# Kernel tuning notes

Hardware: AMD Instinct MI355X
Metric: run time of the kernel (lower is better)

The kernel has to match this reference:

```python
import jax, jax.numpy as jnp
import numpy as np

B, S, D, H, E, K = 8, 512, 512, 1024, 8, 2


def setup_inputs() -> dict:
    key = jax.random.key(0)
    ks = jax.random.split(key, 8)
    x = jax.random.normal(ks[0], (B, S, D), dtype=jnp.float32)
    mask = jax.random.randint(ks[1], (B, S), 0, 2, dtype=jnp.int32)
    # xavier-uniform gate weights (torch init.xavier_uniform_)
    lim_g = np.sqrt(6.0 / (D + E))
    w_gate = jax.random.uniform(ks[2], (D, E), minval=-lim_g, maxval=lim_g, dtype=jnp.float32)
    # per-expert MLP params (nn.Linear default: U(-1/sqrt(fan_in), 1/sqrt(fan_in)))
    lim1 = 1.0 / np.sqrt(D)
    lim2 = 1.0 / np.sqrt(H)
    W1 = jax.random.uniform(ks[3], (E, D, H), minval=-lim1, maxval=lim1, dtype=jnp.float32)
    b1 = jax.random.uniform(ks[4], (E, H), minval=-lim1, maxval=lim1, dtype=jnp.float32)
    W2 = jax.random.uniform(ks[5], (E, H, D), minval=-lim2, maxval=lim2, dtype=jnp.float32)
    b2 = jax.random.uniform(ks[6], (E, D), minval=-lim2, maxval=lim2, dtype=jnp.float32)
    return {"x": x, "mask": mask, "w_gate": w_gate, "W1": W1, "b1": b1, "W2": W2, "b2": b2}


def reference(x, mask, w_gate, W1, b1, W2, b2):
    # --- top-k gating (noisy_gating=False path; loss = 0) ---
    logits = jnp.einsum('bsd,de->bse', x, w_gate)              # [B,S,E]
    top_vals, top_idx = jax.lax.top_k(logits, K)               # [B,S,K]
    top_gates = jax.nn.softmax(top_vals, axis=-1)              # softmax over top-k only
    onehot = jax.nn.one_hot(top_idx, E, dtype=x.dtype)         # [B,S,K,E]
    gates = jnp.einsum('bsk,bske->bse', top_gates, onehot)     # scatter to dense gates
    gates = gates * mask[..., None].astype(x.dtype)            # self.clean(gates, mask)
    # --- per-expert 2-layer MLP, combined with gates ---
    # dense formulation: zero gates contribute zero, identical math to dispatch/combine
    h = jax.nn.relu(jnp.einsum('bsd,edh->besh', x, W1) + b1[None, :, None, :])
    out = jnp.einsum('besh,eho->beso', h, W2) + b2[None, :, None, :]
    y = jnp.einsum('bse,beso->bso', gates, out)
    # dropout is identity in eval; residual add
    return y + x
```

## Files before the change

kernel.cpp:

```cpp
#include <hip/hip_runtime.h>
#include <cmath>

#define B_ 8
#define S_ 512
#define D_ 512
#define H_ 1024
#define E_ 8
#define NT_ (B_*S_)
#define TM 16
#define MAXTILE 40

typedef __attribute__((ext_vector_type(8))) short short8v;
typedef __attribute__((ext_vector_type(4))) float f32x4;

__device__ inline unsigned short f2bf(float f) {
    union { float f; unsigned u; } a; a.f = f;
    unsigned u = a.u;
    return (unsigned short)((u + 0x7FFF + ((u >> 16) & 1)) >> 16);
}
__device__ inline float bf2f(unsigned short u) {
    union { unsigned u; float f; } a; a.u = ((unsigned)u) << 16; return a.f;
}


__global__ __launch_bounds__(256) void prep_fused(
    const float* __restrict__ x, const int* __restrict__ mask,
    const float* __restrict__ wg,
    const float* __restrict__ W1, const float* __restrict__ W2,
    float* __restrict__ out, unsigned short* __restrict__ xbf,
    uchar2* __restrict__ tokE, float2* __restrict__ tokG,
    unsigned short* __restrict__ W1S, unsigned short* __restrict__ W2S)
{
    const int tid = threadIdx.x, wave = tid >> 6, lane = tid & 63;
    const int bid = blockIdx.x;

    if (bid < 1024) {
        const int t = bid * 4 + wave;
        const float4* xr = (const float4*)(x + ((size_t)t << 9));
        const float4 v0 = xr[lane];
        const float4 v1 = xr[lane + 64];
        float4* orow = (float4*)(out + ((size_t)t << 9));
        orow[lane] = v0; orow[lane + 64] = v1;
        union { unsigned short u[4]; uint2 w; } pa, pb;
        pa.u[0]=f2bf(v0.x); pa.u[1]=f2bf(v0.y); pa.u[2]=f2bf(v0.z); pa.u[3]=f2bf(v0.w);
        pb.u[0]=f2bf(v1.x); pb.u[1]=f2bf(v1.y); pb.u[2]=f2bf(v1.z); pb.u[3]=f2bf(v1.w);
        uint2* xrow = (uint2*)(xbf + ((size_t)t << 9));
        xrow[lane] = pa.w; xrow[lane + 64] = pb.w;

        float acc[E_];
#pragma unroll
        for (int e = 0; e < E_; ++e) acc[e] = 0.f;
        const int d0 = lane * 4;
#pragma unroll
        for (int dd = 0; dd < 4; ++dd) {
            const float xa = (&v0.x)[dd], xb = (&v1.x)[dd];
            const float4 wa0 = *(const float4*)(wg + (size_t)(d0 + dd) * 8);
            const float4 wa1 = *(const float4*)(wg + (size_t)(d0 + dd) * 8 + 4);
            const float4 wb0 = *(const float4*)(wg + (size_t)(256 + d0 + dd) * 8);
            const float4 wb1 = *(const float4*)(wg + (size_t)(256 + d0 + dd) * 8 + 4);
            acc[0] += xa * wa0.x + xb * wb0.x;
            acc[1] += xa * wa0.y + xb * wb0.y;
            acc[2] += xa * wa0.z + xb * wb0.z;
            acc[3] += xa * wa0.w + xb * wb0.w;
            acc[4] += xa * wa1.x + xb * wb1.x;
            acc[5] += xa * wa1.y + xb * wb1.y;
            acc[6] += xa * wa1.z + xb * wb1.z;
            acc[7] += xa * wa1.w + xb * wb1.w;
        }
#pragma unroll
        for (int e = 0; e < E_; ++e) {
            float v = acc[e];
#pragma unroll
            for (int off = 32; off > 0; off >>= 1) v += __shfl_xor(v, off, 64);
            acc[e] = v;
        }
        if (lane == 0) {
            if (mask[t] != 0) {
                int i0 = 0; float v0m = acc[0];
#pragma unroll
                for (int e = 1; e < E_; ++e) if (acc[e] > v0m) { v0m = acc[e]; i0 = e; }
                int i1 = -1; float v1m = -INFINITY;
#pragma unroll
                for (int e = 0; e < E_; ++e) if (e != i0 && acc[e] > v1m) { v1m = acc[e]; i1 = e; }
                const float ex = __expf(v1m - v0m);
                const float denom = 1.f + ex;
                tokE[t] = make_uchar2((unsigned char)i0, (unsigned char)i1);
                tokG[t] = make_float2(1.f / denom, ex / denom);
            } else {
                tokE[t] = make_uchar2(255, 255);
            }
        }
        return;
    }

    const int isW2 = (bid >= 1536);
    const int q = ((bid - (isW2 ? 1536 : 1024)) << 2) | wave;
    const int e = q >> 8, rem = q & 255;
    const int g = lane >> 4, m = lane & 15;
    const float* base; unsigned short* dstB; int stride, K32, Fq, kidx;
    if (!isW2) {
        Fq = rem >> 4; kidx = rem & 15;
        stride = H_; K32 = 16; base = W1; dstB = W1S;
    } else {
        Fq = rem >> 5; kidx = rem & 31;
        stride = D_; K32 = 32; base = W2; dstB = W2S;
    }
    const int k = kidx * 32 + g * 8;
    const float* src = base + ((size_t)e << 19) + (size_t)k * stride + Fq * 64 + m;
    float v[4][8];
#pragma unroll
    for (int j = 0; j < 8; ++j) {
#pragma unroll
        for (int c = 0; c < 4; ++c)
            v[c][j] = src[(size_t)j * stride + c * 16];
    }
#pragma unroll
    for (int c = 0; c < 4; ++c) {
        union { unsigned short u[8]; uint4 qv; } p;
#pragma unroll
        for (int j = 0; j < 8; ++j) p.u[j] = f2bf(v[c][j]);
        unsigned short* dst = dstB + ((size_t)e << 19)
                            + ((size_t)((Fq * 4 + c) * K32 + kidx) << 9) + lane * 8;
        *(uint4*)dst = p.qv;
    }
}

__global__ __launch_bounds__(256) void build1_kernel(
    const uchar2* __restrict__ tokE,
    ushort2* __restrict__ locs, int* __restrict__ blockCnt)
{
    __shared__ int waveTot[4][E_];
    const int tid = threadIdx.x, lane = tid & 63, wave = tid >> 6;
    const int t = blockIdx.x * 256 + tid;
    const uchar2 ee = tokE[t];
    int scan_pre[E_];
#pragma unroll
    for (int e = 0; e < E_; ++e) {
        const int orig = (ee.x == e) + (ee.y == e);
        int v = orig;
#pragma unroll
        for (int off = 1; off < 64; off <<= 1) {
            const int o = __shfl_up(v, off, 64);
            if (lane >= off) v += o;
        }
        scan_pre[e] = v - orig;
        if (lane == 63) waveTot[wave][e] = v;
    }
    __syncthreads();
    int loc0 = 0, loc1 = 0;
#pragma unroll
    for (int e = 0; e < E_; ++e) {
        int add = 0;
#pragma unroll
        for (int w = 0; w < 4; ++w) if (w < wave) add += waveTot[w][e];
        const int pre = scan_pre[e] + add;
        if (ee.x == e) loc0 = pre;
        if (ee.y == e) loc1 = pre;
    }
    if (tid < E_)
        blockCnt[blockIdx.x * E_ + tid] =
            waveTot[0][tid] + waveTot[1][tid] + waveTot[2][tid] + waveTot[3][tid];
    if (ee.x != 255)
        locs[t] = make_ushort2((unsigned short)loc0, (unsigned short)loc1);
}

__global__ __launch_bounds__(256) void build2_kernel(
    const uchar2* __restrict__ tokE, const float2* __restrict__ tokG,
    const ushort2* __restrict__ locs, const int* __restrict__ blockCnt,
    int* __restrict__ counts, int* __restrict__ lists, float* __restrict__ gvals,
    ushort2* __restrict__ tokSlot)
{
    __shared__ int bc[16][E_];
    const int tid = threadIdx.x;
    const int b = blockIdx.x;
    if (tid < 16 * E_) bc[tid >> 3][tid & 7] = blockCnt[tid];
    __syncthreads();
    if (b == 0 && tid < E_) {
        int s = 0;
#pragma unroll
        for (int bb = 0; bb < 16; ++bb) s += bc[bb][tid];
        counts[tid] = s;
    }
    const int t = b * 256 + tid;
    const uchar2 ee = tokE[t];
    if (ee.x == 255) return;
    int base0 = 0, base1 = 0, ex0 = 0, ex1 = 0, cum = 0;
#pragma unroll
    for (int e = 0; e < E_; ++e) {
        int boff = 0, tot = 0;
#pragma unroll
        for (int bb = 0; bb < 16; ++bb) {
            const int v = bc[bb][e];
            tot += v;
            if (bb < b) boff += v;
        }
        if (ee.x == e) { base0 = boff; ex0 = cum; }
        if (ee.y == e) { base1 = boff; ex1 = cum; }
        cum += tot;
    }
    const ushort2 lc = locs[t];
    const float2 gg = tokG[t];
    const int s0 = ee.x * NT_ + base0 + lc.x;
    const int s1 = ee.y * NT_ + base1 + lc.y;
    lists[s0] = t; gvals[s0] = gg.x;
    lists[s1] = t; gvals[s1] = gg.y;
    tokSlot[t] = make_ushort2((unsigned short)(ex0 + base0 + lc.x),
                              (unsigned short)(ex1 + base1 + lc.y));
}

__global__ __launch_bounds__(256) void stage1_kernel(
    const unsigned short* __restrict__ xbf,
    const unsigned short* __restrict__ W1S, const float* __restrict__ b1,
    const int* __restrict__ counts, const int* __restrict__ lists,
    unsigned short* __restrict__ Hbuf)
{
    __shared__ int tks[32];
    __shared__ unsigned short Xs[32 * D_];
    char* XsC = (char*)Xs;

    const int bid = blockIdx.x;
    const int e  = bid & 7;
    const int nb = (bid >> 3) & 3;
    const int ti = bid >> 5;
    const int n_e = counts[e];
    const int t0 = ti << 5;
    if (t0 >= n_e) return;
    int off = 0;
#pragma unroll
    for (int i = 0; i < E_; ++i) if (i < e) off += counts[i];
    const int mact = min(32, n_e - t0);
    const int tid = threadIdx.x;
    if (tid < 32) tks[tid] = lists[e * NT_ + t0 + min(tid, mact - 1)];
    __syncthreads();

#pragma unroll
    for (int j = 0; j < 8; ++j) {
        const int idx = tid + j * 256;
        const int row = idx >> 6, c = idx & 63;
        const uint4 v = *(const uint4*)(xbf + ((size_t)tks[row] << 9) + c * 8);
        *(uint4*)(XsC + ((row * 1024 + c * 16) ^ ((row & 7) << 4))) = v;
    }
    __syncthreads();

    const int wave = tid >> 6, lane = tid & 63, m = lane & 15, g = lane >> 4;
    const int colbase = nb * 256 + wave * 64;

    const int aoff0 = m * 1024 + (g << 4);
    const int aoff1 = (16 + m) * 1024 + (g << 4);
    const int aswz  = (m & 7) << 4;
    const unsigned short* Bb = W1S + ((size_t)e << 19)
                             + ((size_t)(nb * 16 + wave * 4) << 13) + (lane << 3);

    f32x4 acc[2][4];
#pragma unroll
    for (int i = 0; i < 2; ++i)
#pragma unroll
        for (int f = 0; f < 4; ++f) acc[i][f] = (f32x4){0.f, 0.f, 0.f, 0.f};

#pragma unroll 2
    for (int kk = 0; kk < 16; ++kk) {
        const short8v a0 = *(const short8v*)(XsC + ((aoff0 + (kk << 6)) ^ aswz));
        const short8v a1 = *(const short8v*)(XsC + ((aoff1 + (kk << 6)) ^ aswz));
        const short8v b0  = *(const short8v*)(Bb + (kk << 9));
        const short8v b1v = *(const short8v*)(Bb + (1 << 13) + (kk << 9));
        const short8v b2v = *(const short8v*)(Bb + (2 << 13) + (kk << 9));
        const short8v b3  = *(const short8v*)(Bb + (3 << 13) + (kk << 9));
        acc[0][0] = __builtin_amdgcn_mfma_f32_16x16x32_bf16(a0, b0,  acc[0][0], 0, 0, 0);
        acc[1][0] = __builtin_amdgcn_mfma_f32_16x16x32_bf16(a1, b0,  acc[1][0], 0, 0, 0);
        acc[0][1] = __builtin_amdgcn_mfma_f32_16x16x32_bf16(a0, b1v, acc[0][1], 0, 0, 0);
        acc[1][1] = __builtin_amdgcn_mfma_f32_16x16x32_bf16(a1, b1v, acc[1][1], 0, 0, 0);
        acc[0][2] = __builtin_amdgcn_mfma_f32_16x16x32_bf16(a0, b2v, acc[0][2], 0, 0, 0);
        acc[1][2] = __builtin_amdgcn_mfma_f32_16x16x32_bf16(a1, b2v, acc[1][2], 0, 0, 0);
        acc[0][3] = __builtin_amdgcn_mfma_f32_16x16x32_bf16(a0, b3,  acc[0][3], 0, 0, 0);
        acc[1][3] = __builtin_amdgcn_mfma_f32_16x16x32_bf16(a1, b3,  acc[1][3], 0, 0, 0);
    }

#pragma unroll
    for (int f = 0; f < 4; ++f) {
        const int col = colbase + f * 16 + m;
        const float bias = b1[(e << 10) + col];
#pragma unroll
        for (int i = 0; i < 2; ++i)
#pragma unroll
            for (int r = 0; r < 4; ++r) {
                const int row = i * 16 + g * 4 + r;
                if (row < mact)
                    Hbuf[((size_t)(off + t0 + row) << 10) + col] =
                        f2bf(fmaxf(acc[i][f][r] + bias, 0.f));
            }
    }
}

__global__ __launch_bounds__(256) void stage2y_kernel(
    const unsigned short* __restrict__ Hbuf,
    const unsigned short* __restrict__ W2S, const float* __restrict__ b2,
    const int* __restrict__ counts, unsigned short* __restrict__ Ybuf)
{
    __shared__ unsigned short Hs[32 * 512];
    char* HsC = (char*)Hs;

    const int bid = blockIdx.x;
    const int e  = bid & 7;
    const int nb = (bid >> 3) & 1;
    const int ti = bid >> 4;
    const int n_e = counts[e];
    const int t0 = ti << 5;
    if (t0 >= n_e) return;
    int off = 0;
#pragma unroll
    for (int i = 0; i < E_; ++i) if (i < e) off += counts[i];
    const int mact = min(32, n_e - t0);

    const int tid = threadIdx.x;
    const int wave = tid >> 6, lane = tid & 63, m = lane & 15, g = lane >> 4;
    const int colbase = nb * 256 + wave * 64;
    const int aswz = (m & 7) << 4;

    const unsigned short* Bb = W2S + ((size_t)e << 19)
                             + ((size_t)(nb * 16 + wave * 4) << 14) + (lane << 3);

    f32x4 acc[2][4];
#pragma unroll
    for (int i = 0; i < 2; ++i)
#pragma unroll
        for (int f = 0; f < 4; ++f) acc[i][f] = (f32x4){0.f, 0.f, 0.f, 0.f};

#pragma unroll
    for (int phase = 0; phase < 2; ++phase) {
        if (phase) __syncthreads();
#pragma unroll
        for (int j = 0; j < 8; ++j) {
            const int idx = tid + j * 256;
            const int row = idx >> 6, c = idx & 63;
            const uint4 v = *(const uint4*)(Hbuf + ((size_t)(off + t0 + row) << 10)
                                            + phase * 512 + c * 8);
            *(uint4*)(HsC + ((row * 1024 + c * 16) ^ ((row & 7) << 4))) = v;
        }
        __syncthreads();

#pragma unroll 2
        for (int kk = 0; kk < 16; ++kk) {
            const short8v a0 = *(const short8v*)(HsC + ((m * 1024 + (kk << 6) + (g << 4)) ^ aswz));
            const short8v a1 = *(const short8v*)(HsC + (((16 + m) * 1024 + (kk << 6) + (g << 4)) ^ aswz));
            const int kg = phase * 16 + kk;
            const short8v b0  = *(const short8v*)(Bb + (kg << 9));
            const short8v b1v = *(const short8v*)(Bb + (1 << 14) + (kg << 9));
            const short8v b2v = *(const short8v*)(Bb + (2 << 14) + (kg << 9));
            const short8v b3  = *(const short8v*)(Bb + (3 << 14) + (kg << 9));
            acc[0][0] = __builtin_amdgcn_mfma_f32_16x16x32_bf16(b0,  a0, acc[0][0], 0, 0, 0);
            acc[1][0] = __builtin_amdgcn_mfma_f32_16x16x32_bf16(b0,  a1, acc[1][0], 0, 0, 0);
            acc[0][1] = __builtin_amdgcn_mfma_f32_16x16x32_bf16(b1v, a0, acc[0][1], 0, 0, 0);
            acc[1][1] = __builtin_amdgcn_mfma_f32_16x16x32_bf16(b1v, a1, acc[1][1], 0, 0, 0);
            acc[0][2] = __builtin_amdgcn_mfma_f32_16x16x32_bf16(b2v, a0, acc[0][2], 0, 0, 0);
            acc[1][2] = __builtin_amdgcn_mfma_f32_16x16x32_bf16(b2v, a1, acc[1][2], 0, 0, 0);
            acc[0][3] = __builtin_amdgcn_mfma_f32_16x16x32_bf16(b3,  a0, acc[0][3], 0, 0, 0);
            acc[1][3] = __builtin_amdgcn_mfma_f32_16x16x32_bf16(b3,  a1, acc[1][3], 0, 0, 0);
        }
    }

#pragma unroll
    for (int f = 0; f < 4; ++f) {
        const int c0 = colbase + f * 16 + 4 * g;
        const float4 bv = *(const float4*)(b2 + (e << 9) + c0);
#pragma unroll
        for (int i = 0; i < 2; ++i) {
            const int token = i * 16 + m;
            if (token < mact) {
                const unsigned lo = (unsigned)f2bf(acc[i][f][0] + bv.x)
                                  | ((unsigned)f2bf(acc[i][f][1] + bv.y) << 16);
                const unsigned hi = (unsigned)f2bf(acc[i][f][2] + bv.z)
                                  | ((unsigned)f2bf(acc[i][f][3] + bv.w) << 16);
                *(uint2*)(Ybuf + ((size_t)(off + t0 + token) << 9) + c0) = make_uint2(lo, hi);
            }
        }
    }
}

__global__ __launch_bounds__(256) void combine_kernel(
    const uchar2* __restrict__ tokE, const float2* __restrict__ tokG,
    const ushort2* __restrict__ tokSlot, const unsigned short* __restrict__ Ybuf,
    float* __restrict__ out)
{
    const int tid = threadIdx.x, wave = tid >> 6, lane = tid & 63;
    const int t = blockIdx.x * 4 + wave;
    const uchar2 ee = tokE[t];
    if (ee.x == 255) return;
    const float2 gg = tokG[t];
    const ushort2 ss = tokSlot[t];
    const unsigned short* y0 = Ybuf + ((size_t)ss.x << 9);
    const unsigned short* y1 = Ybuf + ((size_t)ss.y << 9);
    float4* orow = (float4*)(out + ((size_t)t << 9));
#pragma unroll
    for (int h = 0; h < 2; ++h) {
        const int idx = lane + h * 64;
        float4 o = orow[idx];
        const uint2 a = *(const uint2*)(y0 + 4 * idx);
        const uint2 b = *(const uint2*)(y1 + 4 * idx);
        o.x += gg.x * bf2f((unsigned short)(a.x & 0xFFFF)) + gg.y * bf2f((unsigned short)(b.x & 0xFFFF));
        o.y += gg.x * bf2f((unsigned short)(a.x >> 16))    + gg.y * bf2f((unsigned short)(b.x >> 16));
        o.z += gg.x * bf2f((unsigned short)(a.y & 0xFFFF)) + gg.y * bf2f((unsigned short)(b.y & 0xFFFF));
        o.w += gg.x * bf2f((unsigned short)(a.y >> 16))    + gg.y * bf2f((unsigned short)(b.y >> 16));
        orow[idx] = o;
    }
}

__global__ __launch_bounds__(256) void stage2_kernel(
    const unsigned short* __restrict__ Hbuf,
    const unsigned short* __restrict__ W2S, const float* __restrict__ b2,
    const int* __restrict__ counts, const int* __restrict__ lists,
    const float* __restrict__ gvals, float* __restrict__ out)
{
    const int bid = blockIdx.x;
    const int e  = bid & 7;
    const int nb = (bid >> 3) & 1;
    const int ti = bid >> 4;
    const int n_e = counts[e];
    const int t0 = ti << 5;
    if (t0 >= n_e) return;
    int off = 0;
#pragma unroll
    for (int i = 0; i < E_; ++i) if (i < e) off += counts[i];
    const int mact = min(32, n_e - t0);
    __shared__ int tks[32];
    __shared__ float gsh[32];
    const int tid = threadIdx.x;
    if (tid < 32) {
        const int idx = min(tid, mact - 1);
        tks[tid] = lists[e * NT_ + t0 + idx];
        gsh[tid] = gvals[e * NT_ + t0 + idx];
    }
    __syncthreads();

    const int wave = tid >> 6, lane = tid & 63, m = lane & 15, g = lane >> 4;
    const int colbase = nb * 256 + wave * 64;

    const unsigned short* a0p = Hbuf + ((size_t)(off + t0 + m) << 10) + (g << 3);
    const unsigned short* a1p = Hbuf + ((size_t)(off + t0 + 16 + m) << 10) + (g << 3);
    const unsigned short* Bb = W2S + ((size_t)e << 19)
                             + ((size_t)(nb * 16 + wave * 4) << 14) + (lane << 3);

    f32x4 acc[2][4];
#pragma unroll
    for (int i = 0; i < 2; ++i)
#pragma unroll
        for (int f = 0; f < 4; ++f) acc[i][f] = (f32x4){0.f, 0.f, 0.f, 0.f};

#pragma unroll 2
    for (int kk = 0; kk < 32; ++kk) {
        const short8v a0 = *(const short8v*)(a0p + (kk << 5));
        const short8v a1 = *(const short8v*)(a1p + (kk << 5));
        const short8v b0  = *(const short8v*)(Bb + (kk << 9));
        const short8v b1v = *(const short8v*)(Bb + (1 << 14) + (kk << 9));
        const short8v b2v = *(const short8v*)(Bb + (2 << 14) + (kk << 9));
        const short8v b3  = *(const short8v*)(Bb + (3 << 14) + (kk << 9));
        acc[0][0] = __builtin_amdgcn_mfma_f32_16x16x32_bf16(a0, b0,  acc[0][0], 0, 0, 0);
        acc[1][0] = __builtin_amdgcn_mfma_f32_16x16x32_bf16(a1, b0,  acc[1][0], 0, 0, 0);
        acc[0][1] = __builtin_amdgcn_mfma_f32_16x16x32_bf16(a0, b1v, acc[0][1], 0, 0, 0);
        acc[1][1] = __builtin_amdgcn_mfma_f32_16x16x32_bf16(a1, b1v, acc[1][1], 0, 0, 0);
        acc[0][2] = __builtin_amdgcn_mfma_f32_16x16x32_bf16(a0, b2v, acc[0][2], 0, 0, 0);
        acc[1][2] = __builtin_amdgcn_mfma_f32_16x16x32_bf16(a1, b2v, acc[1][2], 0, 0, 0);
        acc[0][3] = __builtin_amdgcn_mfma_f32_16x16x32_bf16(a0, b3,  acc[0][3], 0, 0, 0);
        acc[1][3] = __builtin_amdgcn_mfma_f32_16x16x32_bf16(a1, b3,  acc[1][3], 0, 0, 0);
    }

#pragma unroll
    for (int f = 0; f < 4; ++f) {
        const int col = colbase + f * 16 + m;
        const float bias = b2[(e << 9) + col];
#pragma unroll
        for (int i = 0; i < 2; ++i)
#pragma unroll
            for (int r = 0; r < 4; ++r) {
                const int row = i * 16 + g * 4 + r;
                if (row < mact)
                    atomicAdd(out + ((size_t)tks[row] << 9) + col,
                              (acc[i][f][r] + bias) * gsh[row]);
            }
    }
}


__global__ __launch_bounds__(256) void gating_kernel(
    const float* __restrict__ x, const int* __restrict__ mask,
    const float* __restrict__ wg, int* __restrict__ counts,
    int* __restrict__ lists, float* __restrict__ gvals)
{
    const int wave = threadIdx.x >> 6;
    const int lane = threadIdx.x & 63;
    const int t = blockIdx.x * 4 + wave;
    const float* xr = x + (size_t)t * D_;
    float acc[E_];
#pragma unroll
    for (int e = 0; e < E_; ++e) acc[e] = 0.f;
    for (int d = lane; d < D_; d += 64) {
        const float xv = xr[d];
        const float* wr = wg + (size_t)d * E_;
#pragma unroll
        for (int e = 0; e < E_; ++e) acc[e] += xv * wr[e];
    }
#pragma unroll
    for (int e = 0; e < E_; ++e) {
        float v = acc[e];
#pragma unroll
        for (int off = 32; off > 0; off >>= 1) v += __shfl_down(v, off, 64);
        acc[e] = v;
    }
    if (lane == 0 && mask[t] != 0) {
        int i0 = 0; float v0 = acc[0];
#pragma unroll
        for (int e = 1; e < E_; ++e) if (acc[e] > v0) { v0 = acc[e]; i0 = e; }
        int i1 = -1; float v1 = -INFINITY;
#pragma unroll
        for (int e = 0; e < E_; ++e) if (e != i0 && acc[e] > v1) { v1 = acc[e]; i1 = e; }
        const float ex = __expf(v1 - v0);
        const float denom = 1.f + ex;
        const int p0 = atomicAdd(&counts[i0], 1);
        lists[i0 * NT_ + p0] = t; gvals[i0 * NT_ + p0] = 1.f / denom;
        const int p1 = atomicAdd(&counts[i1], 1);
        lists[i1 * NT_ + p1] = t; gvals[i1 * NT_ + p1] = ex / denom;
    }
}

__global__ __launch_bounds__(256) void init_out_kernel(
    const float* __restrict__ x, float* __restrict__ out)
{
    const size_t i = (size_t)blockIdx.x * blockDim.x + threadIdx.x;
    ((float4*)out)[i] = ((const float4*)x)[i];
}

__global__ __launch_bounds__(256) void transpose_cvt(
    const float* __restrict__ src, unsigned short* __restrict__ dst, int R, int C)
{
    __shared__ unsigned short t[64][72];
    const float* s = src + (size_t)blockIdx.z * R * C;
    unsigned short* d = dst + (size_t)blockIdx.z * R * C;
    const int r0 = blockIdx.y * 64, c0 = blockIdx.x * 64;
    const int tc = threadIdx.x & 63;
    const int tr = threadIdx.x >> 6;
#pragma unroll
    for (int i = 0; i < 16; ++i) {
        const int r = tr + i * 4;
        t[r][tc] = f2bf(s[(size_t)(r0 + r) * C + c0 + tc]);
    }
    __syncthreads();
    const int c = threadIdx.x >> 2;
    const int ch = threadIdx.x & 3;
#pragma unroll
    for (int half = 0; half < 2; ++half) {
        union { unsigned short u[8]; uint4 v; } p;
#pragma unroll
        for (int k = 0; k < 8; ++k) p.u[k] = t[ch * 16 + half * 8 + k][c];
        *(uint4*)(d + (size_t)(c0 + c) * R + r0 + ch * 16 + half * 8) = p.v;
    }
}

__global__ __launch_bounds__(256) void expert_mfma(
    const float* __restrict__ x,
    const unsigned short* __restrict__ W1T, const float* __restrict__ b1,
    const unsigned short* __restrict__ W2T, const float* __restrict__ b2,
    const int* __restrict__ counts, const int* __restrict__ lists,
    const float* __restrict__ gvals, float* __restrict__ out)
{
    __shared__ unsigned short Xs[TM * D_];
    __shared__ unsigned short Hs2[TM * H_];
    __shared__ int   tks[TM];
    __shared__ float gs[TM];

    const int bi = blockIdx.x;
    const int e = bi & 7;
    const int t0 = (bi >> 3) * TM;
    const int n = counts[e];
    if (t0 >= n) return;
    const int tid = threadIdx.x;
    const int mact = min(TM, n - t0);
    const int wave = tid >> 6;
    const int lane = tid & 63;
    const int m = lane & 15;
    const int g = lane >> 4;
    char* XsC = (char*)Xs;
    char* HsC = (char*)Hs2;

    if (tid < TM) {
        if (tid < mact) {
            tks[tid] = lists[e * NT_ + t0 + tid];
            gs[tid]  = gvals[e * NT_ + t0 + tid];
        } else { tks[tid] = 0; gs[tid] = 0.f; }
    }
    __syncthreads();

    for (int idx = tid; idx < TM * (D_ / 8); idx += 256) {
        const int mm = idx >> 6;
        const int c8 = idx & 63;
        union { unsigned short u[8]; uint4 v; } p;
        if (mm < mact) {
            const float4* xr = (const float4*)(x + (size_t)tks[mm] * D_);
            const float4 v0 = xr[c8 * 2], v1 = xr[c8 * 2 + 1];
            p.u[0]=f2bf(v0.x); p.u[1]=f2bf(v0.y); p.u[2]=f2bf(v0.z); p.u[3]=f2bf(v0.w);
            p.u[4]=f2bf(v1.x); p.u[5]=f2bf(v1.y); p.u[6]=f2bf(v1.z); p.u[7]=f2bf(v1.w);
        } else {
            p.v = make_uint4(0, 0, 0, 0);
        }
        const int off = mm * (D_ * 2) + c8 * 16;
        *(uint4*)(XsC + (off ^ ((mm & 7) << 4))) = p.v;
    }
    __syncthreads();

    const int nbase = wave * 256;
    f32x4 acc1[16];
#pragma unroll
    for (int f = 0; f < 16; ++f) acc1[f] = (f32x4){0.f, 0.f, 0.f, 0.f};

    for (int k0 = 0; k0 < D_; k0 += 32) {
        const int aoff = m * (D_ * 2) + k0 * 2 + g * 16;
        const short8v a = *(const short8v*)(XsC + (aoff ^ ((m & 7) << 4)));
#pragma unroll
        for (int f = 0; f < 16; ++f) {
            const unsigned short* bp = W1T + (((size_t)(e << 10) + nbase + f * 16 + m) << 9) + k0 + g * 8;
            const short8v b = *(const short8v*)bp;
            acc1[f] = __builtin_amdgcn_mfma_f32_16x16x32_bf16(a, b, acc1[f], 0, 0, 0);
        }
    }
#pragma unroll
    for (int f = 0; f < 16; ++f) {
        const int nn = nbase + f * 16 + m;
        const float bias = b1[(e << 10) + nn];
#pragma unroll
        for (int r = 0; r < 4; ++r) {
            const int mm = g * 4 + r;
            const unsigned short hv = f2bf(fmaxf(acc1[f][r] + bias, 0.f));
            const int off = mm * (H_ * 2) + nn * 2;
            *(unsigned short*)(HsC + (off ^ ((mm & 7) << 4))) = hv;
        }
    }
    __syncthreads();

    const int obase = wave * 128;
    f32x4 acc2[8];
#pragma unroll
    for (int f = 0; f < 8; ++f) acc2[f] = (f32x4){0.f, 0.f, 0.f, 0.f};

    for (int k0 = 0; k0 < H_; k0 += 32) {
        const int aoff = m * (H_ * 2) + k0 * 2 + g * 16;
        const short8v a = *(const short8v*)(HsC + (aoff ^ ((m & 7) << 4)));
#pragma unroll
        for (int f = 0; f < 8; ++f) {
            const unsigned short* bp = W2T + (((size_t)(e << 9) + obase + f * 16 + m) << 10) + k0 + g * 8;
            const short8v b = *(const short8v*)bp;
            acc2[f] = __builtin_amdgcn_mfma_f32_16x16x32_bf16(a, b, acc2[f], 0, 0, 0);
        }
    }
#pragma unroll
    for (int f = 0; f < 8; ++f) {
        const int o = obase + f * 16 + m;
        const float bias = b2[(e << 9) + o];
#pragma unroll
        for (int r = 0; r < 4; ++r) {
            const int mm = g * 4 + r;
            const float gv = gs[mm];
            if (gv != 0.f)
                atomicAdd(out + (size_t)tks[mm] * D_ + o, (acc2[f][r] + bias) * gv);
        }
    }
}

__global__ __launch_bounds__(256) void expert_fp32(
    const float* __restrict__ x,
    const float* __restrict__ W1, const float* __restrict__ b1,
    const float* __restrict__ W2, const float* __restrict__ b2,
    const int* __restrict__ counts, const int* __restrict__ lists,
    const float* __restrict__ gvals, float* __restrict__ out)
{
    __shared__ float Xs[TM][D_];
    __shared__ float Hs3[TM][H_];
    __shared__ int   tks[TM];
    __shared__ float gs[TM];

    const int e  = blockIdx.y;
    const int n  = counts[e];
    const int t0 = blockIdx.x * TM;
    if (t0 >= n) return;
    const int tid  = threadIdx.x;
    const int mact = min(TM, n - t0);

    if (tid < TM) {
        if (tid < mact) {
            tks[tid] = lists[e * NT_ + t0 + tid];
            gs[tid]  = gvals[e * NT_ + t0 + tid];
        } else { tks[tid] = 0; gs[tid] = 0.f; }
    }
    __syncthreads();
    for (int idx = tid; idx < TM * (D_ / 4); idx += 256) {
        const int mm = idx >> 7, c = idx & 127;
        float4 v = make_float4(0.f, 0.f, 0.f, 0.f);
        if (mm < mact) v = ((const float4*)(x + (size_t)tks[mm] * D_))[c];
        ((float4*)&Xs[mm][0])[c] = v;
    }
    __syncthreads();
    const float* W1e = W1 + (size_t)e * D_ * H_;
    float acc[4][TM];
#pragma unroll
    for (int jj = 0; jj < 4; ++jj)
#pragma unroll
        for (int mm = 0; mm < TM; ++mm) acc[jj][mm] = 0.f;
    for (int d4 = 0; d4 < D_ / 4; ++d4) {
        float w[4][4];
#pragma unroll
        for (int dd = 0; dd < 4; ++dd) {
            const float* wp = W1e + (size_t)(d4 * 4 + dd) * H_ + tid;
#pragma unroll
            for (int jj = 0; jj < 4; ++jj) w[dd][jj] = wp[jj * 256];
        }
#pragma unroll
        for (int mm = 0; mm < TM; ++mm) {
            const float4 xv = ((const float4*)&Xs[mm][0])[d4];
            const float* xp = &xv.x;
#pragma unroll
            for (int dd = 0; dd < 4; ++dd)
#pragma unroll
                for (int jj = 0; jj < 4; ++jj)
                    acc[jj][mm] = fmaf(xp[dd], w[dd][jj], acc[jj][mm]);
        }
    }
#pragma unroll
    for (int jj = 0; jj < 4; ++jj) {
        const int j = jj * 256 + tid;
        const float bv = b1[e * H_ + j];
#pragma unroll
        for (int mm = 0; mm < TM; ++mm) Hs3[mm][j] = fmaxf(acc[jj][mm] + bv, 0.f);
    }
    __syncthreads();
    const float* W2e = W2 + (size_t)e * H_ * D_;
    float acc2[2][TM];
#pragma unroll
    for (int oo = 0; oo < 2; ++oo)
#pragma unroll
        for (int mm = 0; mm < TM; ++mm) acc2[oo][mm] = 0.f;
    for (int j4 = 0; j4 < H_ / 4; ++j4) {
        float w[4][2];
#pragma unroll
        for (int dd = 0; dd < 4; ++dd) {
            const float* wp = W2e + (size_t)(j4 * 4 + dd) * D_ + tid;
#pragma unroll
            for (int oo = 0; oo < 2; ++oo) w[dd][oo] = wp[oo * 256];
        }
#pragma unroll
        for (int mm = 0; mm < TM; ++mm) {
            const float4 hv = ((const float4*)&Hs3[mm][0])[j4];
            const float* hp = &hv.x;
#pragma unroll
            for (int dd = 0; dd < 4; ++dd)
#pragma unroll
                for (int oo = 0; oo < 2; ++oo)
                    acc2[oo][mm] = fmaf(hp[dd], w[dd][oo], acc2[oo][mm]);
        }
    }
#pragma unroll
    for (int oo = 0; oo < 2; ++oo) {
        const int o = oo * 256 + tid;
        const float bv = b2[e * D_ + o];
        for (int mm = 0; mm < mact; ++mm)
            atomicAdd(out + (size_t)tks[mm] * D_ + o, (acc2[oo][mm] + bv) * gs[mm]);
    }
}


extern "C" void kernel_launch(void* const* d_in, const int* in_sizes, int n_in,
                              void* d_out, int out_size, void* d_ws, size_t ws_size,
                              hipStream_t stream)
{
    const float* x    = (const float*)d_in[0];
    const int*   mask = (const int*)d_in[1];
    const float* wg   = (const float*)d_in[2];
    const float* W1   = (const float*)d_in[3];
    const float* b1   = (const float*)d_in[4];
    const float* W2   = (const float*)d_in[5];
    const float* b2   = (const float*)d_in[6];
    float* out = (float*)d_out;

    char* ws = (char*)d_ws;
    int*   counts = (int*)ws;
    int*   lists  = (int*)(ws + 256);
    float* gvals  = (float*)(ws + 256 + 131072);

    ushort2* tokSlot = (ushort2*)(ws + 0x42000);
    uchar2* tokE = (uchar2*)(ws + 0x48000);
    float2* tokG = (float2*)(ws + 0x50000);
    ushort2* locs = (ushort2*)(ws + 0x58000);
    int* blockCnt = (int*)(ws + 0x5C000);
    unsigned short* xbf  = (unsigned short*)(ws + 0x60000);
    unsigned short* W1Sa = (unsigned short*)(ws + 0x480000);
    unsigned short* W2Sa = (unsigned short*)(ws + 0xC80000);
    unsigned short* Hbuf = (unsigned short*)(ws + 0x1480000);
    unsigned short* Ybuf = (unsigned short*)(ws + 0x2500000);
    const size_t needA  = 0x2500000;
    const size_t needA2 = 0x2500000 + (size_t)8448 * 512 * 2;

    const size_t wt_bytes = (size_t)E_ * D_ * H_ * 2;
    const size_t needB = 524288 + 2 * wt_bytes;

    if (ws_size >= needA) {
        prep_fused<<<2048, 256, 0, stream>>>(x, mask, wg, W1, W2,
                                             out, xbf, tokE, tokG, W1Sa, W2Sa);
        build1_kernel<<<16, 256, 0, stream>>>(tokE, locs, blockCnt);
        build2_kernel<<<16, 256, 0, stream>>>(tokE, tokG, locs, blockCnt,
                                              counts, lists, gvals, tokSlot);
        stage1_kernel<<<MAXTILE * 4 * 8, 256, 0, stream>>>(xbf, W1Sa, b1, counts, lists, Hbuf);
        if (ws_size >= needA2) {
            stage2y_kernel<<<MAXTILE * 2 * 8, 256, 0, stream>>>(Hbuf, W2Sa, b2, counts, Ybuf);
            combine_kernel<<<1024, 256, 0, stream>>>(tokE, tokG, tokSlot, Ybuf, out);
        } else {
            stage2_kernel<<<MAXTILE * 2 * 8, 256, 0, stream>>>(Hbuf, W2Sa, b2, counts, lists, gvals, out);
        }
    } else if (ws_size >= needB) {
        unsigned short* W1T = (unsigned short*)(ws + 524288);
        unsigned short* W2T = (unsigned short*)(ws + 524288 + wt_bytes);
        hipMemsetAsync(counts, 0, E_ * sizeof(int), stream);
        gating_kernel<<<NT_ / 4, 256, 0, stream>>>(x, mask, wg, counts, lists, gvals);
        init_out_kernel<<<(NT_ * D_) / 4 / 256, 256, 0, stream>>>(x, out);
        transpose_cvt<<<dim3(H_ / 64, D_ / 64, E_), 256, 0, stream>>>(W1, W1T, D_, H_);
        transpose_cvt<<<dim3(D_ / 64, H_ / 64, E_), 256, 0, stream>>>(W2, W2T, H_, D_);
        expert_mfma<<<(NT_ / TM) * E_, 256, 0, stream>>>(x, W1T, b1, W2T, b2,
                                                         counts, lists, gvals, out);
    } else {
        hipMemsetAsync(counts, 0, E_ * sizeof(int), stream);
        gating_kernel<<<NT_ / 4, 256, 0, stream>>>(x, mask, wg, counts, lists, gvals);
        init_out_kernel<<<(NT_ * D_) / 4 / 256, 256, 0, stream>>>(x, out);
        expert_fp32<<<dim3(NT_ / TM, E_), 256, 0, stream>>>(x, W1, b1, W2, b2,
                                                            counts, lists, gvals, out);
    }
}
```

Measured before the change: 63.10 us.

## Merge routing build kernels and move residual copy into combine

Result: slower. 67.35 us (+6.7%).

```diff
diff --git a/kernel.cpp b/kernel.cpp
--- a/kernel.cpp
+++ b/kernel.cpp
@@ -27,7 +27,7 @@
     const float* __restrict__ x, const int* __restrict__ mask,
     const float* __restrict__ wg,
     const float* __restrict__ W1, const float* __restrict__ W2,
-    float* __restrict__ out, unsigned short* __restrict__ xbf,
+    unsigned short* __restrict__ xbf,
     uchar2* __restrict__ tokE, float2* __restrict__ tokG,
     unsigned short* __restrict__ W1S, unsigned short* __restrict__ W2S)
 {
@@ -39,8 +39,6 @@
         const float4* xr = (const float4*)(x + ((size_t)t << 9));
         const float4 v0 = xr[lane];
         const float4 v1 = xr[lane + 64];
-        float4* orow = (float4*)(out + ((size_t)t << 9));
-        orow[lane] = v0; orow[lane + 64] = v1;
         union { unsigned short u[4]; uint2 w; } pa, pb;
         pa.u[0]=f2bf(v0.x); pa.u[1]=f2bf(v0.y); pa.u[2]=f2bf(v0.z); pa.u[3]=f2bf(v0.w);
         pb.u[0]=f2bf(v1.x); pb.u[1]=f2bf(v1.y); pb.u[2]=f2bf(v1.z); pb.u[3]=f2bf(v1.w);
@@ -125,14 +123,41 @@
     }
 }
 
-__global__ __launch_bounds__(256) void build1_kernel(
-    const uchar2* __restrict__ tokE,
-    ushort2* __restrict__ locs, int* __restrict__ blockCnt)
-{
+__global__ __launch_bounds__(256) void build_kernel(
+    const uchar2* __restrict__ tokE, const float2* __restrict__ tokG,
+    int* __restrict__ counts, int* __restrict__ lists, float* __restrict__ gvals,
+    ushort2* __restrict__ tokSlot)
+{
+    __shared__ int wAll[4][E_];
+    __shared__ int wPre[4][E_];
     __shared__ int waveTot[4][E_];
     const int tid = threadIdx.x, lane = tid & 63, wave = tid >> 6;
-    const int t = blockIdx.x * 256 + tid;
-    const uchar2 ee = tokE[t];
+    const int b = blockIdx.x;
+
+    int hAll[E_], hPre[E_];
+#pragma unroll
+    for (int e = 0; e < E_; ++e) { hAll[e] = 0; hPre[e] = 0; }
+    for (int bb = 0; bb < 16; ++bb) {
+        const uchar2 e2 = tokE[bb * 256 + tid];
+#pragma unroll
+        for (int e = 0; e < E_; ++e) {
+            const int c = (e2.x == e) + (e2.y == e);
+            hAll[e] += c;
+            if (bb < b) hPre[e] += c;
+        }
+    }
+#pragma unroll
+    for (int e = 0; e < E_; ++e) {
+        int va = hAll[e], vp = hPre[e];
+#pragma unroll
+        for (int off = 32; off > 0; off >>= 1) {
+            va += __shfl_xor(va, off, 64);
+            vp += __shfl_xor(vp, off, 64);
+        }
+        if (lane == 0) { wAll[wave][e] = va; wPre[wave][e] = vp; }
+    }
+
+    const uchar2 ee = tokE[b * 256 + tid];
     int scan_pre[E_];
 #pragma unroll
     for (int e = 0; e < E_; ++e) {
@@ -147,65 +172,35 @@
         if (lane == 63) waveTot[wave][e] = v;
     }
     __syncthreads();
-    int loc0 = 0, loc1 = 0;
+
+    int tot[E_], boff[E_];
 #pragma unroll
     for (int e = 0; e < E_; ++e) {
-        int add = 0;
+        tot[e]  = wAll[0][e] + wAll[1][e] + wAll[2][e] + wAll[3][e];
+        boff[e] = wPre[0][e] + wPre[1][e] + wPre[2][e] + wPre[3][e];
+    }
+    if (b == 0 && tid < E_) counts[tid] = tot[tid];
+
+    if (ee.x == 255) return;
+    int we0 = 0, we1 = 0, ex0 = 0, ex1 = 0, cum = 0;
+#pragma unroll
+    for (int e = 0; e < E_; ++e) {
+        int add = boff[e];
 #pragma unroll
         for (int w = 0; w < 4; ++w) if (w < wave) add += waveTot[w][e];
         const int pre = scan_pre[e] + add;
-        if (ee.x == e) loc0 = pre;
-        if (ee.y == e) loc1 = pre;
-    }
-    if (tid < E_)
-        blockCnt[blockIdx.x * E_ + tid] =
-            waveTot[0][tid] + waveTot[1][tid] + waveTot[2][tid] + waveTot[3][tid];
-    if (ee.x != 255)
-        locs[t] = make_ushort2((unsigned short)loc0, (unsigned short)loc1);
-}
-
-__global__ __launch_bounds__(256) void build2_kernel(
-    const uchar2* __restrict__ tokE, const float2* __restrict__ tokG,
-    const ushort2* __restrict__ locs, const int* __restrict__ blockCnt,
-    int* __restrict__ counts, int* __restrict__ lists, float* __restrict__ gvals,
-    ushort2* __restrict__ tokSlot)
-{
-    __shared__ int bc[16][E_];
-    const int tid = threadIdx.x;
-    const int b = blockIdx.x;
-    if (tid < 16 * E_) bc[tid >> 3][tid & 7] = blockCnt[tid];
-    __syncthreads();
-    if (b == 0 && tid < E_) {
-        int s = 0;
-#pragma unroll
-        for (int bb = 0; bb < 16; ++bb) s += bc[bb][tid];
-        counts[tid] = s;
-    }
+        if (ee.x == e) { we0 = pre; ex0 = cum; }
+        if (ee.y == e) { we1 = pre; ex1 = cum; }
+        cum += tot[e];
+    }
+    const float2 gg = tokG[b * 256 + tid];
     const int t = b * 256 + tid;
-    const uchar2 ee = tokE[t];
-    if (ee.x == 255) return;
-    int base0 = 0, base1 = 0, ex0 = 0, ex1 = 0, cum = 0;
-#pragma unroll
-    for (int e = 0; e < E_; ++e) {
-        int boff = 0, tot = 0;
-#pragma unroll
-        for (int bb = 0; bb < 16; ++bb) {
-            const int v = bc[bb][e];
-            tot += v;
-            if (bb < b) boff += v;
-        }
-        if (ee.x == e) { base0 = boff; ex0 = cum; }
-        if (ee.y == e) { base1 = boff; ex1 = cum; }
-        cum += tot;
-    }
-    const ushort2 lc = locs[t];
-    const float2 gg = tokG[t];
-    const int s0 = ee.x * NT_ + base0 + lc.x;
-    const int s1 = ee.y * NT_ + base1 + lc.y;
+    const int s0 = ee.x * NT_ + we0;
+    const int s1 = ee.y * NT_ + we1;
     lists[s0] = t; gvals[s0] = gg.x;
     lists[s1] = t; gvals[s1] = gg.y;
-    tokSlot[t] = make_ushort2((unsigned short)(ex0 + base0 + lc.x),
-                              (unsigned short)(ex1 + base1 + lc.y));
+    tokSlot[t] = make_ushort2((unsigned short)(ex0 + we0),
+                              (unsigned short)(ex1 + we1));
 }
 
 __global__ __launch_bounds__(256) void stage1_kernel(
@@ -377,6 +372,7 @@
 }
 
 __global__ __launch_bounds__(256) void combine_kernel(
+    const float* __restrict__ x,
     const uchar2* __restrict__ tokE, const float2* __restrict__ tokG,
     const ushort2* __restrict__ tokSlot, const unsigned short* __restrict__ Ybuf,
     float* __restrict__ out)
@@ -384,16 +380,21 @@
     const int tid = threadIdx.x, wave = tid >> 6, lane = tid & 63;
     const int t = blockIdx.x * 4 + wave;
     const uchar2 ee = tokE[t];
-    if (ee.x == 255) return;
+    const float4* xrow = (const float4*)(x + ((size_t)t << 9));
+    float4* orow = (float4*)(out + ((size_t)t << 9));
+    if (ee.x == 255) {
+        orow[lane] = xrow[lane];
+        orow[lane + 64] = xrow[lane + 64];
+        return;
+    }
     const float2 gg = tokG[t];
     const ushort2 ss = tokSlot[t];
     const unsigned short* y0 = Ybuf + ((size_t)ss.x << 9);
     const unsigned short* y1 = Ybuf + ((size_t)ss.y << 9);
-    float4* orow = (float4*)(out + ((size_t)t << 9));
 #pragma unroll
     for (int h = 0; h < 2; ++h) {
         const int idx = lane + h * 64;
-        float4 o = orow[idx];
+        float4 o = xrow[idx];
         const uint2 a = *(const uint2*)(y0 + 4 * idx);
         const uint2 b = *(const uint2*)(y1 + 4 * idx);
         o.x += gg.x * bf2f((unsigned short)(a.x & 0xFFFF)) + gg.y * bf2f((unsigned short)(b.x & 0xFFFF));
@@ -401,81 +402,6 @@
         o.z += gg.x * bf2f((unsigned short)(a.y & 0xFFFF)) + gg.y * bf2f((unsigned short)(b.y & 0xFFFF));
         o.w += gg.x * bf2f((unsigned short)(a.y >> 16))    + gg.y * bf2f((unsigned short)(b.y >> 16));
         orow[idx] = o;
-    }
-}
-
-__global__ __launch_bounds__(256) void stage2_kernel(
-    const unsigned short* __restrict__ Hbuf,
-    const unsigned short* __restrict__ W2S, const float* __restrict__ b2,
-    const int* __restrict__ counts, const int* __restrict__ lists,
-    const float* __restrict__ gvals, float* __restrict__ out)
-{
-    const int bid = blockIdx.x;
-    const int e  = bid & 7;
-    const int nb = (bid >> 3) & 1;
-    const int ti = bid >> 4;
-    const int n_e = counts[e];
-    const int t0 = ti << 5;
-    if (t0 >= n_e) return;
-    int off = 0;
-#pragma unroll
-    for (int i = 0; i < E_; ++i) if (i < e) off += counts[i];
-    const int mact = min(32, n_e - t0);
-    __shared__ int tks[32];
-    __shared__ float gsh[32];
-    const int tid = threadIdx.x;
-    if (tid < 32) {
-        const int idx = min(tid, mact - 1);
-        tks[tid] = lists[e * NT_ + t0 + idx];
-        gsh[tid] = gvals[e * NT_ + t0 + idx];
-    }
-    __syncthreads();
-
-    const int wave = tid >> 6, lane = tid & 63, m = lane & 15, g = lane >> 4;
-    const int colbase = nb * 256 + wave * 64;
-
-    const unsigned short* a0p = Hbuf + ((size_t)(off + t0 + m) << 10) + (g << 3);
-    const unsigned short* a1p = Hbuf + ((size_t)(off + t0 + 16 + m) << 10) + (g << 3);
-    const unsigned short* Bb = W2S + ((size_t)e << 19)
-                             + ((size_t)(nb * 16 + wave * 4) << 14) + (lane << 3);
-
-    f32x4 acc[2][4];
-#pragma unroll
-    for (int i = 0; i < 2; ++i)
-#pragma unroll
-        for (int f = 0; f < 4; ++f) acc[i][f] = (f32x4){0.f, 0.f, 0.f, 0.f};
-
-#pragma unroll 2
-    for (int kk = 0; kk < 32; ++kk) {
-        const short8v a0 = *(const short8v*)(a0p + (kk << 5));
-        const short8v a1 = *(const short8v*)(a1p + (kk << 5));
-        const short8v b0  = *(const short8v*)(Bb + (kk << 9));
-        const short8v b1v = *(const short8v*)(Bb + (1 << 14) + (kk << 9));
-        const short8v b2v = *(const short8v*)(Bb + (2 << 14) + (kk << 9));
-        const short8v b3  = *(const short8v*)(Bb + (3 << 14) + (kk << 9));
-        acc[0][0] = __builtin_amdgcn_mfma_f32_16x16x32_bf16(a0, b0,  acc[0][0], 0, 0, 0);
-        acc[1][0] = __builtin_amdgcn_mfma_f32_16x16x32_bf16(a1, b0,  acc[1][0], 0, 0, 0);
-        acc[0][1] = __builtin_amdgcn_mfma_f32_16x16x32_bf16(a0, b1v, acc[0][1], 0, 0, 0);
-        acc[1][1] = __builtin_amdgcn_mfma_f32_16x16x32_bf16(a1, b1v, acc[1][1], 0, 0, 0);
-        acc[0][2] = __builtin_amdgcn_mfma_f32_16x16x32_bf16(a0, b2v, acc[0][2], 0, 0, 0);
-        acc[1][2] = __builtin_amdgcn_mfma_f32_16x16x32_bf16(a1, b2v, acc[1][2], 0, 0, 0);
-        acc[0][3] = __builtin_amdgcn_mfma_f32_16x16x32_bf16(a0, b3,  acc[0][3], 0, 0, 0);
-        acc[1][3] = __builtin_amdgcn_mfma_f32_16x16x32_bf16(a1, b3,  acc[1][3], 0, 0, 0);
-    }
-
-#pragma unroll
-    for (int f = 0; f < 4; ++f) {
-        const int col = colbase + f * 16 + m;
-        const float bias = b2[(e << 9) + col];
-#pragma unroll
-        for (int i = 0; i < 2; ++i)
-#pragma unroll
-            for (int r = 0; r < 4; ++r) {
-                const int row = i * 16 + g * 4 + r;
-                if (row < mact)
-                    atomicAdd(out + ((size_t)tks[row] << 9) + col,
-                              (acc[i][f][r] + bias) * gsh[row]);
-            }
     }
 }
 
@@ -785,32 +711,23 @@
     ushort2* tokSlot = (ushort2*)(ws + 0x42000);
     uchar2* tokE = (uchar2*)(ws + 0x48000);
     float2* tokG = (float2*)(ws + 0x50000);
-    ushort2* locs = (ushort2*)(ws + 0x58000);
-    int* blockCnt = (int*)(ws + 0x5C000);
     unsigned short* xbf  = (unsigned short*)(ws + 0x60000);
     unsigned short* W1Sa = (unsigned short*)(ws + 0x480000);
     unsigned short* W2Sa = (unsigned short*)(ws + 0xC80000);
     unsigned short* Hbuf = (unsigned short*)(ws + 0x1480000);
     unsigned short* Ybuf = (unsigned short*)(ws + 0x2500000);
-    const size_t needA  = 0x2500000;
     const size_t needA2 = 0x2500000 + (size_t)8448 * 512 * 2;
 
     const size_t wt_bytes = (size_t)E_ * D_ * H_ * 2;
     const size_t needB = 524288 + 2 * wt_bytes;
 
-    if (ws_size >= needA) {
+    if (ws_size >= needA2) {
         prep_fused<<<2048, 256, 0, stream>>>(x, mask, wg, W1, W2,
-                                             out, xbf, tokE, tokG, W1Sa, W2Sa);
-        build1_kernel<<<16, 256, 0, stream>>>(tokE, locs, blockCnt);
-        build2_kernel<<<16, 256, 0, stream>>>(tokE, tokG, locs, blockCnt,
-                                              counts, lists, gvals, tokSlot);
+                                             xbf, tokE, tokG, W1Sa, W2Sa);
+        build_kernel<<<16, 256, 0, stream>>>(tokE, tokG, counts, lists, gvals, tokSlot);
         stage1_kernel<<<MAXTILE * 4 * 8, 256, 0, stream>>>(xbf, W1Sa, b1, counts, lists, Hbuf);
-        if (ws_size >= needA2) {
-            stage2y_kernel<<<MAXTILE * 2 * 8, 256, 0, stream>>>(Hbuf, W2Sa, b2, counts, Ybuf);
-            combine_kernel<<<1024, 256, 0, stream>>>(tokE, tokG, tokSlot, Ybuf, out);
-        } else {
-            stage2_kernel<<<MAXTILE * 2 * 8, 256, 0, stream>>>(Hbuf, W2Sa, b2, counts, lists, gvals, out);
-        }
+        stage2y_kernel<<<MAXTILE * 2 * 8, 256, 0, stream>>>(Hbuf, W2Sa, b2, counts, Ybuf);
+        combine_kernel<<<1024, 256, 0, stream>>>(x, tokE, tokG, tokSlot, Ybuf, out);
     } else if (ws_size >= needB) {
         unsigned short* W1T = (unsigned short*)(ws + 524288);
         unsigned short* W2T = (unsigned short*)(ws + 524288 + wt_bytes);
```
